# Kernel optimization log

Hardware: AMD Instinct MI355X
Metric: run time of the kernel (lower is better)

The kernel has to match this reference:

```python
import jax, jax.numpy as jnp
import numpy as np

D_HEAD = 64  # d_adapter // n_heads with n_heads=1

def setup_inputs() -> dict:
    key = jax.random.key(0)
    ks = jax.random.split(key, 7)
    L, B, S, D = 8, 2, 4096, 2048
    N, Ds, Da = 128, 1024, 64
    g = 0.1  # xavier gain used in init (only affects scale; use plain normals scaled similarly)
    return {
        "hidden": jax.random.normal(ks[0], (L, B, S, D), jnp.float32),
        "bank": jax.random.normal(ks[1], (B, N, Ds), jnp.float32),
        "Wq": jax.random.normal(ks[2], (L, Da, D), jnp.float32) * (g / np.sqrt(D)),
        "Wk": jax.random.normal(ks[3], (L, Da, Ds), jnp.float32) * (g / np.sqrt(Ds)),
        "Wv": jax.random.normal(ks[4], (L, Da, Ds), jnp.float32) * (g / np.sqrt(Ds)),
        "Wo": jax.random.normal(ks[5], (L, D, Da), jnp.float32) * (g / np.sqrt(Da)),
        "gates": jnp.full((L,), -2.0, jnp.float32),
    }

def reference(hidden, bank, Wq, Wk, Wv, Wo, gates):
    # hidden: (L,B,S,D) per-layer hidden states; bank: (B,N,Ds) shared summary bank
    h = hidden.astype(jnp.float32)
    bk = bank.astype(jnp.float32)
    Q = jnp.einsum('lbsd,lad->lbsa', h, Wq)        # (L,B,S,Da)
    K = jnp.einsum('bnc,lac->lbna', bk, Wk)        # (L,B,N,Da)
    V = jnp.einsum('bnc,lac->lbna', bk, Wv)        # (L,B,N,Da)
    scale = 1.0 / jnp.sqrt(jnp.asarray(D_HEAD, jnp.float32))
    scores = jnp.einsum('lbsa,lbna->lbsn', Q, K) * scale
    attn = jax.nn.softmax(scores, axis=-1)          # (L,B,S,N)
    attn_out = jnp.einsum('lbsn,lbna->lbsa', attn, V)
    resid = jnp.einsum('lbsa,lda->lbsd', attn_out, Wo)
    gate = jax.nn.sigmoid(gates)[:, None, None, None]
    return hidden + (gate * resid).astype(hidden.dtype)
```

## Files before the change

kernel.cpp:

```cpp
#include <hip/hip_runtime.h>
#include <cstdint>
#include <cstddef>


typedef __attribute__((ext_vector_type(8))) short short8;
typedef __attribute__((ext_vector_type(4))) float f32x4;
typedef __attribute__((ext_vector_type(4))) unsigned short u16x4;

#define MFMA16(a, b, c) __builtin_amdgcn_mfma_f32_16x16x32_bf16((a), (b), (c), 0, 0, 0)

__device__ __forceinline__ unsigned short f2bf(float f) {
  unsigned int x = __builtin_bit_cast(unsigned int, f);
  x += 0x7fffu + ((x >> 16) & 1u);
  return (unsigned short)(x >> 16);
}
__device__ __forceinline__ float bf2f(unsigned short u) {
  return __builtin_bit_cast(float, (unsigned int)u << 16);
}
__device__ __forceinline__ short8 cvt8v(f32x4 a, f32x4 b) {
  short8 r;
  r[0] = (short)f2bf(a[0]); r[1] = (short)f2bf(a[1]);
  r[2] = (short)f2bf(a[2]); r[3] = (short)f2bf(a[3]);
  r[4] = (short)f2bf(b[0]); r[5] = (short)f2bf(b[1]);
  r[6] = (short)f2bf(b[2]); r[7] = (short)f2bf(b[3]);
  return r;
}
__device__ __forceinline__ short8 ld_cvt8(const float* p) {
  f32x4 v0 = *(const f32x4*)p, v1 = *(const f32x4*)(p + 4);
  return cvt8v(v0, v1);
}
__device__ __forceinline__ u16x4 pack4(f32x4 v) {
  u16x4 r;
  r[0] = f2bf(v[0]); r[1] = f2bf(v[1]); r[2] = f2bf(v[2]); r[3] = f2bf(v[3]);
  return r;
}

__global__ __launch_bounds__(64)
void pre_kv_kernel(const float* __restrict__ bank,
                   const float* __restrict__ Wk,
                   const float* __restrict__ Wv,
                   unsigned short* __restrict__ KF, unsigned short* __restrict__ VF) {
  int bid = blockIdx.x;
  int at = bid & 3, nt = (bid >> 2) & 7, kv = (bid >> 5) & 1;
  int b = (bid >> 6) & 1, l = bid >> 7;
  int lane = threadIdx.x & 63;
  int lo = lane & 15, hi = lane >> 4;
  const float* W  = (kv ? Wv : Wk) + (size_t)l * 65536;
  const float* bk = bank + (size_t)b * 131072;
  int lbq = l * 2 + b;
  f32x4 acc = (f32x4){0.f, 0.f, 0.f, 0.f};
  for (int ks = 0; ks < 32; ++ks) {
    short8 A = ld_cvt8(bk + (nt * 16 + lo) * 1024 + ks * 32 + hi * 8);
    short8 B = ld_cvt8(W + (at * 16 + lo) * 1024 + ks * 32 + hi * 8);
    acc = MFMA16(A, B, acc);
  }
  for (int r = 0; r < 4; ++r) {
    int n = nt * 16 + hi * 4 + r;
    int a = at * 16 + lo;
    unsigned short v = f2bf(acc[r]);
    if (kv == 0) {
      int idx = ((lbq * 8 + (n >> 4)) * 2 + (a >> 5)) * 512 +
                (((a >> 3) & 3) * 16 + (n & 15)) * 8 + (a & 7);
      KF[idx] = v;
    } else {
      int idx = ((lbq * 4 + (a >> 4)) * 4 + (n >> 5)) * 512 +
                (((n >> 3) & 3) * 16 + (a & 15)) * 8 + (n & 7);
      VF[idx] = v;
    }
  }
}

__global__ void pre_frag_kernel(const float* __restrict__ Wq, const float* __restrict__ Wo,
                                unsigned short* __restrict__ WqF, unsigned short* __restrict__ WoF) {
  int idx = blockIdx.x * 256 + threadIdx.x;
  if (idx < 131072) {
    int t = idx;
    int lane = t & 63, ks = (t >> 6) & 63, at = (t >> 12) & 3, l = t >> 14;
    int a = at * 16 + (lane & 15), d = ks * 32 + (lane >> 4) * 8;
    *(short8*)(WqF + (size_t)t * 8) = ld_cvt8(Wq + ((size_t)(l * 64 + a)) * 2048 + d);
  } else {
    int t = idx - 131072;
    int lane = t & 63, ks = (t >> 6) & 1, dt = (t >> 7) & 127, l = t >> 14;
    int d = dt * 16 + (lane & 15), a = ks * 32 + (lane >> 4) * 8;
    *(short8*)(WoF + (size_t)t * 8) = ld_cvt8(Wo + ((size_t)(l * 2048 + d)) * 64 + a);
  }
}

__global__ __launch_bounds__(256, 6)
void adapter_main(const float* __restrict__ hidden,
                  const unsigned short* __restrict__ KF, const unsigned short* __restrict__ VF,
                  const unsigned short* __restrict__ WqF, const unsigned short* __restrict__ WoF,
                  const float* __restrict__ gates, float* __restrict__ out) {
  __shared__ __align__(16) char smem[24832];
  float* qsc = (float*)smem;
  unsigned short* Pb = (unsigned short*)(smem + 4352);
  float* aob = (float*)(smem + 8704);
  float* scb = (float*)(smem + 16384);
  char* resb = smem + 16384;

  int bid0 = blockIdx.x;
  int bid = (bid0 & 7) * 512 + (bid0 >> 3);
  int st = bid & 255, b = (bid >> 8) & 1, l = bid >> 9;
  int tid = threadIdx.x, wave = tid >> 6, lane = tid & 63;
  int lo = lane & 15, hi = lane >> 4;
  size_t hbase = ((size_t)(l * 2 + b) * 4096 + st * 16) * 2048;
  const char* hby = (const char*)(hidden + hbase);
  float gate = 1.0f / (1.0f + __expf(-gates[l]));
  int lb = l * 2 + b;
  int at = wave;

  f32x4 sreg[4];
  f32x4 qacc = (f32x4){0.f, 0.f, 0.f, 0.f};
  {
    const unsigned short* wqb = WqF + ((size_t)(l * 4 + at) * 64) * 512 + lane * 8;

#define LOADC(c)                                                             \
    _Pragma("unroll")                                                        \
    for (int s2 = 0; s2 < 4; ++s2) {                                         \
      int row = s2 * 4 + wave;                                               \
      sreg[s2] = *(const f32x4*)(hby + (size_t)row * 8192 + (size_t)(c) * 1024 + lane * 16); \
    }
#define WRITEC(c)                                                            \
    _Pragma("unroll")                                                        \
    for (int s2 = 0; s2 < 4; ++s2) {                                         \
      int row = s2 * 4 + wave;                                               \
      u16x4 pk = pack4(sreg[s2]);                                            \
      *(u16x4*)(smem + ((c) & 1) * 8192 + row * 512 + ((lane * 8) ^ ((row & 7) << 4))) = pk; \
    }

    LOADC(0); WRITEC(0);
    #pragma unroll 1
    for (int c = 0; c < 8; ++c) {
      __syncthreads();
      if (c < 7) LOADC(c + 1);
      const char* rb = smem + (c & 1) * 8192 + lo * 512;
      int sw = (lo & 7) << 4;
      #pragma unroll
      for (int ks = 0; ks < 8; ++ks) {
        short8 A = *(const short8*)(rb + ((ks * 64 + hi * 16) ^ sw));
        short8 B = *(const short8*)(wqb + (size_t)(c * 8 + ks) * 512);
        qacc = MFMA16(A, B, qacc);
      }
      if (c < 7) WRITEC(c + 1);
    }
#undef LOADC
#undef WRITEC
  }

  #pragma unroll
  for (int r = 0; r < 4; ++r)
    qsc[(hi * 4 + r) * 68 + at * 16 + lo] = qacc[r] * 0.125f;
  __syncthreads();

  {
    short8 afrag[2];
    #pragma unroll
    for (int ks = 0; ks < 2; ++ks) {
      const float* qp = qsc + lo * 68 + ks * 32 + hi * 8;
      afrag[ks] = cvt8v(*(const f32x4*)qp, *(const f32x4*)(qp + 4));
    }
    #pragma unroll
    for (int i = 0; i < 2; ++i) {
      int nt = wave * 2 + i;
      f32x4 acc = (f32x4){0.f, 0.f, 0.f, 0.f};
      const unsigned short* kf = KF + ((size_t)(lb * 8 + nt) * 2) * 512 + lane * 8;
      acc = MFMA16(afrag[0], *(const short8*)(kf), acc);
      acc = MFMA16(afrag[1], *(const short8*)(kf + 512), acc);
      #pragma unroll
      for (int r = 0; r < 4; ++r)
        scb[(hi * 4 + r) * 132 + nt * 16 + lo] = acc[r];
    }
  }
  __syncthreads();

  {
    int row = wave * 4 + hi;
    const float* sp = scb + row * 132 + lo * 8;
    f32x4 v0 = *(const f32x4*)sp, v1 = *(const f32x4*)(sp + 4);
    float m = fmaxf(fmaxf(fmaxf(v0[0], v0[1]), fmaxf(v0[2], v0[3])),
                    fmaxf(fmaxf(v1[0], v1[1]), fmaxf(v1[2], v1[3])));
    m = fmaxf(m, __shfl_xor(m, 1)); m = fmaxf(m, __shfl_xor(m, 2));
    m = fmaxf(m, __shfl_xor(m, 4)); m = fmaxf(m, __shfl_xor(m, 8));
    f32x4 e0, e1; float s = 0.f;
    #pragma unroll
    for (int j = 0; j < 4; ++j) { e0[j] = __expf(v0[j] - m); s += e0[j]; }
    #pragma unroll
    for (int j = 0; j < 4; ++j) { e1[j] = __expf(v1[j] - m); s += e1[j]; }
    s += __shfl_xor(s, 1); s += __shfl_xor(s, 2);
    s += __shfl_xor(s, 4); s += __shfl_xor(s, 8);
    float inv = 1.0f / s;
    #pragma unroll
    for (int j = 0; j < 4; ++j) { e0[j] *= inv; e1[j] *= inv; }
    *(short8*)((char*)Pb + row * 272 + lo * 16) = cvt8v(e0, e1);
  }
  __syncthreads();

  {
    short8 pfrag[4];
    #pragma unroll
    for (int ks = 0; ks < 4; ++ks)
      pfrag[ks] = *(const short8*)((const char*)Pb + lo * 272 + ks * 64 + hi * 16);
    const unsigned short* vf = VF + ((size_t)(lb * 4 + at) * 4) * 512 + lane * 8;
    f32x4 a = (f32x4){0.f, 0.f, 0.f, 0.f};
    #pragma unroll
    for (int ks = 0; ks < 4; ++ks)
      a = MFMA16(pfrag[ks], *(const short8*)(vf + (size_t)ks * 512), a);
    #pragma unroll
    for (int r = 0; r < 4; ++r)
      aob[(hi * 4 + r) * 68 + at * 16 + lo] = a[r];
  }
  __syncthreads();

  {
    short8 bfrag[2];
    #pragma unroll
    for (int ks = 0; ks < 2; ++ks) {
      const float* ap2 = aob + lo * 68 + ks * 32 + hi * 8;
      bfrag[ks] = cvt8v(*(const f32x4*)ap2, *(const f32x4*)(ap2 + 4));
    }
    float* ob = out + hbase;
    #pragma unroll 1
    for (int c = 0; c < 8; ++c) {
      #pragma unroll
      for (int j = 0; j < 4; ++j) {
        int dtl = wave * 4 + j;
        int dt = c * 16 + dtl;
        const unsigned short* wo = WoF + ((size_t)(l * 128 + dt) * 2) * 512 + lane * 8;
        short8 A0 = *(const short8*)(wo);
        short8 A1 = *(const short8*)(wo + 512);
        f32x4 acc = (f32x4){0.f, 0.f, 0.f, 0.f};
        acc = MFMA16(A0, bfrag[0], acc);
        acc = MFMA16(A1, bfrag[1], acc);
        *(u16x4*)(resb + lo * 520 + dtl * 32 + hi * 8) = pack4(acc);
      }
      __syncthreads();
      #pragma unroll
      for (int i2 = 0; i2 < 4; ++i2) {
        int row = i2 * 4 + wave;
        size_t off = (size_t)row * 8192 + (size_t)c * 1024 + lane * 16;
        f32x4 hv = *(const f32x4*)(hby + off);
        u16x4 rv = *(const u16x4*)(resb + row * 520 + lane * 8);
        f32x4 o;
        #pragma unroll
        for (int r = 0; r < 4; ++r) o[r] = hv[r] + gate * bf2f(rv[r]);
        __builtin_nontemporal_store(o, (f32x4*)((char*)ob + off));
      }
      __syncthreads();
    }
  }
}

extern "C" void kernel_launch(void* const* d_in, const int* in_sizes, int n_in,
                              void* d_out, int out_size, void* d_ws, size_t ws_size,
                              hipStream_t stream) {
  const float* hidden = (const float*)d_in[0];
  const float* bank   = (const float*)d_in[1];
  const float* Wq     = (const float*)d_in[2];
  const float* Wk     = (const float*)d_in[3];
  const float* Wv     = (const float*)d_in[4];
  const float* Wo     = (const float*)d_in[5];
  const float* gates  = (const float*)d_in[6];
  float* out = (float*)d_out;

  char* ws = (char*)d_ws;
  unsigned short* KF  = (unsigned short*)(ws);
  unsigned short* VF  = (unsigned short*)(ws + 262144);
  unsigned short* WqF = (unsigned short*)(ws + 524288);
  unsigned short* WoF = (unsigned short*)(ws + 2621440);

  pre_kv_kernel<<<1024, 64, 0, stream>>>(bank, Wk, Wv, KF, VF);
  pre_frag_kernel<<<1024, 256, 0, stream>>>(Wq, Wo, WqF, WoF);
  adapter_main<<<4096, 256, 0, stream>>>(hidden, KF, VF, WqF, WoF, gates, out);
}
```

Baseline: 307.2 us.

## Deepen hidden-state prefetch pipelines in Q projection and residual epilogue

The Q-projection loop now uses two register buffers so global loads for chunk c+2 are issued while chunk c+1 is written to LDS and chunk c is consumed, giving a deeper prefetch. The epilogue prefetches the next hidden chunk into registers right after the barrier, overlapping its global reads with the current chunk's stores. It replaces __syncthreads with an explicit lgkmcnt wait plus s_barrier so outstanding vector-memory ops are not drained, and changes the qsc row stride from 68 to 66. The cost is more register pressure, an extra barrier after the Q loop, and the risk that the new qsc stride misaligns the f32x4 reads.

```diff
diff --git a/kernel.cpp b/kernel.cpp
--- a/kernel.cpp
+++ b/kernel.cpp
@@ -109,30 +109,36 @@
   int lb = l * 2 + b;
   int at = wave;
 
-  f32x4 sreg[4];
+  f32x4 sregA[4], sregB[4];
   f32x4 qacc = (f32x4){0.f, 0.f, 0.f, 0.f};
   {
     const unsigned short* wqb = WqF + ((size_t)(l * 4 + at) * 64) * 512 + lane * 8;
 
-#define LOADC(c)                                                             \
+#define LOADC(c, dst)                                                        \
     _Pragma("unroll")                                                        \
     for (int s2 = 0; s2 < 4; ++s2) {                                         \
       int row = s2 * 4 + wave;                                               \
-      sreg[s2] = *(const f32x4*)(hby + (size_t)row * 8192 + (size_t)(c) * 1024 + lane * 16); \
-    }
-#define WRITEC(c)                                                            \
+      dst[s2] = *(const f32x4*)(hby + (size_t)row * 8192 + (size_t)(c) * 1024 + lane * 16); \
+    }
+#define WRITEC(c, src)                                                       \
     _Pragma("unroll")                                                        \
     for (int s2 = 0; s2 < 4; ++s2) {                                         \
       int row = s2 * 4 + wave;                                               \
-      u16x4 pk = pack4(sreg[s2]);                                            \
+      u16x4 pk = pack4(src[s2]);                                             \
       *(u16x4*)(smem + ((c) & 1) * 8192 + row * 512 + ((lane * 8) ^ ((row & 7) << 4))) = pk; \
     }
 
-    LOADC(0); WRITEC(0);
+    LOADC(0, sregA); WRITEC(0, sregA); LOADC(1, sregB);
     #pragma unroll 1
     for (int c = 0; c < 8; ++c) {
       __syncthreads();
-      if (c < 7) LOADC(c + 1);
+      if ((c & 1) == 0) {
+        if (c < 6) LOADC(c + 2, sregA);
+        if (c < 7) WRITEC(c + 1, sregB);
+      } else {
+        if (c < 6) LOADC(c + 2, sregB);
+        if (c < 7) WRITEC(c + 1, sregA);
+      }
       const char* rb = smem + (c & 1) * 8192 + lo * 512;
       int sw = (lo & 7) << 4;
       #pragma unroll
@@ -141,22 +147,22 @@
         short8 B = *(const short8*)(wqb + (size_t)(c * 8 + ks) * 512);
         qacc = MFMA16(A, B, qacc);
       }
-      if (c < 7) WRITEC(c + 1);
     }
 #undef LOADC
 #undef WRITEC
   }
+  __syncthreads();
 
   #pragma unroll
   for (int r = 0; r < 4; ++r)
-    qsc[(hi * 4 + r) * 68 + at * 16 + lo] = qacc[r] * 0.125f;
+    qsc[(hi * 4 + r) * 66 + at * 16 + lo] = qacc[r] * 0.125f;
   __syncthreads();
 
   {
     short8 afrag[2];
     #pragma unroll
     for (int ks = 0; ks < 2; ++ks) {
-      const float* qp = qsc + lo * 68 + ks * 32 + hi * 8;
+      const float* qp = qsc + lo * 66 + ks * 32 + hi * 8;
       afrag[ks] = cvt8v(*(const f32x4*)qp, *(const f32x4*)(qp + 4));
     }
     #pragma unroll
@@ -218,35 +224,57 @@
       const float* ap2 = aob + lo * 68 + ks * 32 + hi * 8;
       bfrag[ks] = cvt8v(*(const f32x4*)ap2, *(const f32x4*)(ap2 + 4));
     }
-    float* ob = out + hbase;
+    char* ob = (char*)(out + hbase);
+    f32x4 hA[4], hB[4];
+
+#define HPREF(c, dst)                                                        \
+    _Pragma("unroll")                                                        \
+    for (int i2 = 0; i2 < 4; ++i2) {                                         \
+      int row = i2 * 4 + wave;                                               \
+      dst[i2] = *(const f32x4*)(hby + (size_t)row * 8192 + (size_t)(c) * 1024 + lane * 16); \
+    }
+#define P5CHUNK(c, hcur, hnext)                                              \
+    do {                                                                     \
+      _Pragma("unroll")                                                      \
+      for (int j = 0; j < 4; ++j) {                                          \
+        int dtl = wave * 4 + j;                                              \
+        int dt = (c) * 16 + dtl;                                             \
+        const unsigned short* wo = WoF + ((size_t)(l * 128 + dt) * 2) * 512 + lane * 8; \
+        short8 A0 = *(const short8*)(wo);                                    \
+        short8 A1 = *(const short8*)(wo + 512);                              \
+        f32x4 acc = (f32x4){0.f, 0.f, 0.f, 0.f};                             \
+        acc = MFMA16(A0, bfrag[0], acc);                                     \
+        acc = MFMA16(A1, bfrag[1], acc);                                     \
+        *(u16x4*)(resb + lo * 520 + dtl * 32 + hi * 8) = pack4(acc);         \
+      }                                                                      \
+      asm volatile("s_waitcnt lgkmcnt(0)" ::: "memory");                     \
+      __builtin_amdgcn_s_barrier();                                          \
+      __builtin_amdgcn_sched_barrier(0);                                     \
+      if ((c) < 7) HPREF((c) + 1, hnext);                                    \
+      _Pragma("unroll")                                                      \
+      for (int i2 = 0; i2 < 4; ++i2) {                                       \
+        int row = i2 * 4 + wave;                                             \
+        size_t off = (size_t)row * 8192 + (size_t)(c) * 1024 + lane * 16;    \
+        u16x4 rv = *(const u16x4*)(resb + row * 520 + lane * 8);             \
+        f32x4 o;                                                             \
+        _Pragma("unroll")                                                    \
+        for (int r = 0; r < 4; ++r) o[r] = hcur[i2][r] + gate * bf2f(rv[r]); \
+        __builtin_nontemporal_store(o, (f32x4*)(ob + off));                  \
+      }                                                                      \
+      asm volatile("s_waitcnt lgkmcnt(0)" ::: "memory");                     \
+      __builtin_amdgcn_s_barrier();                                          \
+      __builtin_amdgcn_sched_barrier(0);                                     \
+    } while (0)
+
+    HPREF(0, hA);
     #pragma unroll 1
-    for (int c = 0; c < 8; ++c) {
-      #pragma unroll
-      for (int j = 0; j < 4; ++j) {
-        int dtl = wave * 4 + j;
-        int dt = c * 16 + dtl;
-        const unsigned short* wo = WoF + ((size_t)(l * 128 + dt) * 2) * 512 + lane * 8;
-        short8 A0 = *(const short8*)(wo);
-        short8 A1 = *(const short8*)(wo + 512);
-        f32x4 acc = (f32x4){0.f, 0.f, 0.f, 0.f};
-        acc = MFMA16(A0, bfrag[0], acc);
-        acc = MFMA16(A1, bfrag[1], acc);
-        *(u16x4*)(resb + lo * 520 + dtl * 32 + hi * 8) = pack4(acc);
-      }
-      __syncthreads();
-      #pragma unroll
-      for (int i2 = 0; i2 < 4; ++i2) {
-        int row = i2 * 4 + wave;
-        size_t off = (size_t)row * 8192 + (size_t)c * 1024 + lane * 16;
-        f32x4 hv = *(const f32x4*)(hby + off);
-        u16x4 rv = *(const u16x4*)(resb + row * 520 + lane * 8);
-        f32x4 o;
-        #pragma unroll
-        for (int r = 0; r < 4; ++r) o[r] = hv[r] + gate * bf2f(rv[r]);
-        __builtin_nontemporal_store(o, (f32x4*)((char*)ob + off));
-      }
-      __syncthreads();
-    }
+    for (int p = 0; p < 4; ++p) {
+      int c = 2 * p;
+      P5CHUNK(c, hA, hB);
+      P5CHUNK(c + 1, hB, hA);
+    }
+#undef HPREF
+#undef P5CHUNK
   }
 }
 
```

Result: slower. 389.5 us (+26.8%).

## Process two row tiles per block, overlapping tile B's Q projection with tile A's output

Applied to the files above, without the earlier changes.

Each block now handles two 16-row tiles. The hidden-state loads and Q-projection MFMAs of the second tile are interleaved with the output projection and residual store of the first tile. The aim is to hide the global-memory stalls of the output phase behind the next tile's load and compute, and to halve the grid to 2048 blocks. In exchange, register pressure goes up, the launch has fewer blocks, and each block's shared-memory use becomes more serialized.

```diff
diff --git a/kernel.cpp b/kernel.cpp
--- a/kernel.cpp
+++ b/kernel.cpp
@@ -99,26 +99,28 @@
   char* resb = smem + 16384;
 
   int bid0 = blockIdx.x;
-  int bid = (bid0 & 7) * 512 + (bid0 >> 3);
-  int st = bid & 255, b = (bid >> 8) & 1, l = bid >> 9;
+  int bid = (bid0 & 7) * 256 + (bid0 >> 3);
+  int p = bid & 127, b = (bid >> 7) & 1, l = bid >> 8;
   int tid = threadIdx.x, wave = tid >> 6, lane = tid & 63;
   int lo = lane & 15, hi = lane >> 4;
-  size_t hbase = ((size_t)(l * 2 + b) * 4096 + st * 16) * 2048;
-  const char* hby = (const char*)(hidden + hbase);
+  size_t hbaseA = ((size_t)(l * 2 + b) * 4096 + p * 32) * 2048;
+  size_t hbaseB = hbaseA + 16 * 2048;
+  const char* hbyA = (const char*)(hidden + hbaseA);
+  const char* hbyB = (const char*)(hidden + hbaseB);
+  char* obA = (char*)(out + hbaseA);
+  char* obB = (char*)(out + hbaseB);
   float gate = 1.0f / (1.0f + __expf(-gates[l]));
   int lb = l * 2 + b;
   int at = wave;
 
   f32x4 sreg[4];
-  f32x4 qacc = (f32x4){0.f, 0.f, 0.f, 0.f};
-  {
-    const unsigned short* wqb = WqF + ((size_t)(l * 4 + at) * 64) * 512 + lane * 8;
-
-#define LOADC(c)                                                             \
+  const unsigned short* wqb = WqF + ((size_t)(l * 4 + at) * 64) * 512 + lane * 8;
+
+#define LOADC(hby, c)                                                        \
     _Pragma("unroll")                                                        \
     for (int s2 = 0; s2 < 4; ++s2) {                                         \
       int row = s2 * 4 + wave;                                               \
-      sreg[s2] = *(const f32x4*)(hby + (size_t)row * 8192 + (size_t)(c) * 1024 + lane * 16); \
+      sreg[s2] = *(const f32x4*)((hby) + (size_t)row * 8192 + (size_t)(c) * 1024 + lane * 16); \
     }
 #define WRITEC(c)                                                            \
     _Pragma("unroll")                                                        \
@@ -128,88 +130,144 @@
       *(u16x4*)(smem + ((c) & 1) * 8192 + row * 512 + ((lane * 8) ^ ((row & 7) << 4))) = pk; \
     }
 
-    LOADC(0); WRITEC(0);
+  auto mid_phases = [&](f32x4 qacc) {
+    #pragma unroll
+    for (int r = 0; r < 4; ++r)
+      qsc[(hi * 4 + r) * 68 + at * 16 + lo] = qacc[r] * 0.125f;
+    __syncthreads();
+    {
+      short8 afrag[2];
+      #pragma unroll
+      for (int ks = 0; ks < 2; ++ks) {
+        const float* qp = qsc + lo * 68 + ks * 32 + hi * 8;
+        afrag[ks] = cvt8v(*(const f32x4*)qp, *(const f32x4*)(qp + 4));
+      }
+      #pragma unroll
+      for (int i = 0; i < 2; ++i) {
+        int nt = wave * 2 + i;
+        f32x4 acc = (f32x4){0.f, 0.f, 0.f, 0.f};
+        const unsigned short* kf = KF + ((size_t)(lb * 8 + nt) * 2) * 512 + lane * 8;
+        acc = MFMA16(afrag[0], *(const short8*)(kf), acc);
+        acc = MFMA16(afrag[1], *(const short8*)(kf + 512), acc);
+        #pragma unroll
+        for (int r = 0; r < 4; ++r)
+          scb[(hi * 4 + r) * 132 + nt * 16 + lo] = acc[r];
+      }
+    }
+    __syncthreads();
+    {
+      int row = wave * 4 + hi;
+      const float* sp = scb + row * 132 + lo * 8;
+      f32x4 v0 = *(const f32x4*)sp, v1 = *(const f32x4*)(sp + 4);
+      float m = fmaxf(fmaxf(fmaxf(v0[0], v0[1]), fmaxf(v0[2], v0[3])),
+                      fmaxf(fmaxf(v1[0], v1[1]), fmaxf(v1[2], v1[3])));
+      m = fmaxf(m, __shfl_xor(m, 1)); m = fmaxf(m, __shfl_xor(m, 2));
+      m = fmaxf(m, __shfl_xor(m, 4)); m = fmaxf(m, __shfl_xor(m, 8));
+      f32x4 e0, e1; float s = 0.f;
+      #pragma unroll
+      for (int j = 0; j < 4; ++j) { e0[j] = __expf(v0[j] - m); s += e0[j]; }
+      #pragma unroll
+      for (int j = 0; j < 4; ++j) { e1[j] = __expf(v1[j] - m); s += e1[j]; }
+      s += __shfl_xor(s, 1); s += __shfl_xor(s, 2);
+      s += __shfl_xor(s, 4); s += __shfl_xor(s, 8);
+      float inv = 1.0f / s;
+      #pragma unroll
+      for (int j = 0; j < 4; ++j) { e0[j] *= inv; e1[j] *= inv; }
+      *(short8*)((char*)Pb + row * 272 + lo * 16) = cvt8v(e0, e1);
+    }
+    __syncthreads();
+    {
+      short8 pfrag[4];
+      #pragma unroll
+      for (int ks = 0; ks < 4; ++ks)
+        pfrag[ks] = *(const short8*)((const char*)Pb + lo * 272 + ks * 64 + hi * 16);
+      const unsigned short* vf = VF + ((size_t)(lb * 4 + at) * 4) * 512 + lane * 8;
+      f32x4 a = (f32x4){0.f, 0.f, 0.f, 0.f};
+      #pragma unroll
+      for (int ks = 0; ks < 4; ++ks)
+        a = MFMA16(pfrag[ks], *(const short8*)(vf + (size_t)ks * 512), a);
+      #pragma unroll
+      for (int r = 0; r < 4; ++r)
+        aob[(hi * 4 + r) * 68 + at * 16 + lo] = a[r];
+    }
+    __syncthreads();
+  };
+
+  f32x4 qaccA = (f32x4){0.f, 0.f, 0.f, 0.f};
+  {
+    LOADC(hbyA, 0); WRITEC(0);
     #pragma unroll 1
     for (int c = 0; c < 8; ++c) {
       __syncthreads();
-      if (c < 7) LOADC(c + 1);
+      if (c < 7) LOADC(hbyA, c + 1);
       const char* rb = smem + (c & 1) * 8192 + lo * 512;
       int sw = (lo & 7) << 4;
       #pragma unroll
       for (int ks = 0; ks < 8; ++ks) {
         short8 A = *(const short8*)(rb + ((ks * 64 + hi * 16) ^ sw));
         short8 B = *(const short8*)(wqb + (size_t)(c * 8 + ks) * 512);
-        qacc = MFMA16(A, B, qacc);
+        qaccA = MFMA16(A, B, qaccA);
       }
       if (c < 7) WRITEC(c + 1);
     }
-#undef LOADC
-#undef WRITEC
-  }
-
+  }
+  __syncthreads();
+
+  mid_phases(qaccA);
+
+  short8 bfragA[2];
   #pragma unroll
-  for (int r = 0; r < 4; ++r)
-    qsc[(hi * 4 + r) * 68 + at * 16 + lo] = qacc[r] * 0.125f;
-  __syncthreads();
-
+  for (int ks = 0; ks < 2; ++ks) {
+    const float* ap2 = aob + lo * 68 + ks * 32 + hi * 8;
+    bfragA[ks] = cvt8v(*(const f32x4*)ap2, *(const f32x4*)(ap2 + 4));
+  }
+  LOADC(hbyB, 0); WRITEC(0);
+
+  f32x4 qaccB = (f32x4){0.f, 0.f, 0.f, 0.f};
   {
-    short8 afrag[2];
-    #pragma unroll
-    for (int ks = 0; ks < 2; ++ks) {
-      const float* qp = qsc + lo * 68 + ks * 32 + hi * 8;
-      afrag[ks] = cvt8v(*(const f32x4*)qp, *(const f32x4*)(qp + 4));
-    }
-    #pragma unroll
-    for (int i = 0; i < 2; ++i) {
-      int nt = wave * 2 + i;
-      f32x4 acc = (f32x4){0.f, 0.f, 0.f, 0.f};
-      const unsigned short* kf = KF + ((size_t)(lb * 8 + nt) * 2) * 512 + lane * 8;
-      acc = MFMA16(afrag[0], *(const short8*)(kf), acc);
-      acc = MFMA16(afrag[1], *(const short8*)(kf + 512), acc);
-      #pragma unroll
-      for (int r = 0; r < 4; ++r)
-        scb[(hi * 4 + r) * 132 + nt * 16 + lo] = acc[r];
-    }
-  }
-  __syncthreads();
-
-  {
-    int row = wave * 4 + hi;
-    const float* sp = scb + row * 132 + lo * 8;
-    f32x4 v0 = *(const f32x4*)sp, v1 = *(const f32x4*)(sp + 4);
-    float m = fmaxf(fmaxf(fmaxf(v0[0], v0[1]), fmaxf(v0[2], v0[3])),
-                    fmaxf(fmaxf(v1[0], v1[1]), fmaxf(v1[2], v1[3])));
-    m = fmaxf(m, __shfl_xor(m, 1)); m = fmaxf(m, __shfl_xor(m, 2));
-    m = fmaxf(m, __shfl_xor(m, 4)); m = fmaxf(m, __shfl_xor(m, 8));
-    f32x4 e0, e1; float s = 0.f;
-    #pragma unroll
-    for (int j = 0; j < 4; ++j) { e0[j] = __expf(v0[j] - m); s += e0[j]; }
-    #pragma unroll
-    for (int j = 0; j < 4; ++j) { e1[j] = __expf(v1[j] - m); s += e1[j]; }
-    s += __shfl_xor(s, 1); s += __shfl_xor(s, 2);
-    s += __shfl_xor(s, 4); s += __shfl_xor(s, 8);
-    float inv = 1.0f / s;
-    #pragma unroll
-    for (int j = 0; j < 4; ++j) { e0[j] *= inv; e1[j] *= inv; }
-    *(short8*)((char*)Pb + row * 272 + lo * 16) = cvt8v(e0, e1);
-  }
-  __syncthreads();
-
-  {
-    short8 pfrag[4];
-    #pragma unroll
-    for (int ks = 0; ks < 4; ++ks)
-      pfrag[ks] = *(const short8*)((const char*)Pb + lo * 272 + ks * 64 + hi * 16);
-    const unsigned short* vf = VF + ((size_t)(lb * 4 + at) * 4) * 512 + lane * 8;
-    f32x4 a = (f32x4){0.f, 0.f, 0.f, 0.f};
-    #pragma unroll
-    for (int ks = 0; ks < 4; ++ks)
-      a = MFMA16(pfrag[ks], *(const short8*)(vf + (size_t)ks * 512), a);
-    #pragma unroll
-    for (int r = 0; r < 4; ++r)
-      aob[(hi * 4 + r) * 68 + at * 16 + lo] = a[r];
-  }
-  __syncthreads();
+    #pragma unroll 1
+    for (int c = 0; c < 8; ++c) {
+      #pragma unroll
+      for (int j = 0; j < 4; ++j) {
+        int dtl = wave * 4 + j;
+        int dt = c * 16 + dtl;
+        const unsigned short* wo = WoF + ((size_t)(l * 128 + dt) * 2) * 512 + lane * 8;
+        short8 A0 = *(const short8*)(wo);
+        short8 A1 = *(const short8*)(wo + 512);
+        f32x4 acc = (f32x4){0.f, 0.f, 0.f, 0.f};
+        acc = MFMA16(A0, bfragA[0], acc);
+        acc = MFMA16(A1, bfragA[1], acc);
+        *(u16x4*)(resb + lo * 520 + dtl * 32 + hi * 8) = pack4(acc);
+      }
+      __syncthreads();
+      if (c < 7) LOADC(hbyB, c + 1);
+      #pragma unroll
+      for (int i2 = 0; i2 < 4; ++i2) {
+        int row = i2 * 4 + wave;
+        size_t off = (size_t)row * 8192 + (size_t)c * 1024 + lane * 16;
+        f32x4 hv = *(const f32x4*)(hbyA + off);
+        u16x4 rv = *(const u16x4*)(resb + row * 520 + lane * 8);
+        f32x4 o;
+        #pragma unroll
+        for (int r = 0; r < 4; ++r) o[r] = hv[r] + gate * bf2f(rv[r]);
+        __builtin_nontemporal_store(o, (f32x4*)(obA + off));
+      }
+      if (c < 7) WRITEC(c + 1);
+      {
+        const char* rb = smem + (c & 1) * 8192 + lo * 512;
+        int sw = (lo & 7) << 4;
+        #pragma unroll
+        for (int ks = 0; ks < 8; ++ks) {
+          short8 A = *(const short8*)(rb + ((ks * 64 + hi * 16) ^ sw));
+          short8 B = *(const short8*)(wqb + (size_t)(c * 8 + ks) * 512);
+          qaccB = MFMA16(A, B, qaccB);
+        }
+      }
+      __syncthreads();
+    }
+  }
+
+  mid_phases(qaccB);
 
   {
     short8 bfrag[2];
@@ -218,7 +276,6 @@
       const float* ap2 = aob + lo * 68 + ks * 32 + hi * 8;
       bfrag[ks] = cvt8v(*(const f32x4*)ap2, *(const f32x4*)(ap2 + 4));
     }
-    float* ob = out + hbase;
     #pragma unroll 1
     for (int c = 0; c < 8; ++c) {
       #pragma unroll
@@ -238,16 +295,18 @@
       for (int i2 = 0; i2 < 4; ++i2) {
         int row = i2 * 4 + wave;
         size_t off = (size_t)row * 8192 + (size_t)c * 1024 + lane * 16;
-        f32x4 hv = *(const f32x4*)(hby + off);
+        f32x4 hv = *(const f32x4*)(hbyB + off);
         u16x4 rv = *(const u16x4*)(resb + row * 520 + lane * 8);
         f32x4 o;
         #pragma unroll
         for (int r = 0; r < 4; ++r) o[r] = hv[r] + gate * bf2f(rv[r]);
-        __builtin_nontemporal_store(o, (f32x4*)((char*)ob + off));
-      }
-      __syncthreads();
-    }
-  }
+        __builtin_nontemporal_store(o, (f32x4*)(obB + off));
+      }
+      __syncthreads();
+    }
+  }
+#undef LOADC
+#undef WRITEC
 }
 
 extern "C" void kernel_launch(void* const* d_in, const int* in_sizes, int n_in,
@@ -270,5 +329,5 @@
 
   pre_kv_kernel<<<1024, 64, 0, stream>>>(bank, Wk, Wv, KF, VF);
   pre_frag_kernel<<<1024, 256, 0, stream>>>(Wq, Wo, WqF, WoF);
-  adapter_main<<<4096, 256, 0, stream>>>(hidden, KF, VF, WqF, WoF, gates, out);
-}
+  adapter_main<<<2048, 256, 0, stream>>>(hidden, KF, VF, WqF, WoF, gates, out);
+}
```

Measured after the change: 404.6 us. +31.7%, slower.
